# Optimization experiments

Measured on AMD Instinct MI355X. Metric: run time of the kernel, lower is better.

Reference implementation:

```python
import jax, jax.numpy as jnp
import numpy as np
from jax import lax

V, E, H, T = 100000, 256, 256, 8192
FL, FN, NC = 5, 128, 20


def setup_inputs() -> dict:
    key = jax.random.key(0)
    ks = jax.random.split(key, 12)
    s = 0.05
    return {
        "docs": jax.random.randint(ks[0], (1, T), 0, V),
        "docs_length": jnp.array([T]),
        "labels": jax.random.randint(ks[1], (1,), 0, NC),
        "iteration": 0,
        "embed_W": jax.random.uniform(ks[2], (V, E), jnp.float32, -0.1, 0.1),
        "w_ih": jax.random.normal(ks[3], (4 * H, E), jnp.float32) * s,
        "w_hh": jax.random.normal(ks[4], (4 * H, H), jnp.float32) * s,
        "b_ih": jax.random.normal(ks[5], (4 * H,), jnp.float32) * s,
        "b_hh": jax.random.normal(ks[6], (4 * H,), jnp.float32) * s,
        "conv_w": jax.random.normal(ks[7], (FN, 1, FL, H), jnp.float32) * s,
        "conv_b": jax.random.normal(ks[8], (FN,), jnp.float32) * s,
        "logits_w": jax.random.uniform(ks[9], (NC, FN), jnp.float32, -0.1, 0.1),
        "logits_b": jnp.zeros((NC,), jnp.float32),
    }


def _forward(docs, labels, embed_W, w_ih, w_hh, b_ih, b_hh, conv_w, conv_b, logits_w, logits_b):
    # embed -> ReLU (dropout is identity at p=0)
    x = jax.nn.relu(embed_W[docs[0]])  # (T, E)

    b = b_ih + b_hh

    def step(carry, xt):
        h, c = carry
        g = xt @ w_ih.T + h @ w_hh.T + b  # (4H,)
        i, f, gg, o = jnp.split(g, 4)
        i = jax.nn.sigmoid(i)
        f = jax.nn.sigmoid(f)
        gg = jnp.tanh(gg)
        o = jax.nn.sigmoid(o)
        c = f * c + i * gg
        h = o * jnp.tanh(c)
        return (h, c), h

    init = (jnp.zeros((H,), x.dtype), jnp.zeros((H,), x.dtype))
    _, hs = lax.scan(step, init, x)  # (T, H)

    # Conv2d(1, FN, (FL, H)) valid: (1,1,T,H) -> (1,FN,T-FL+1,1)
    feat = lax.conv_general_dilated(
        hs[None, None, :, :], conv_w, window_strides=(1, 1), padding="VALID",
        dimension_numbers=("NCHW", "OIHW", "NCHW"))
    feat = feat[0, :, :, 0] + conv_b[:, None]  # (FN, T-FL+1)

    # AdaptiveMaxPool2d((FN,1)) == max over time
    pooled = jnp.max(feat, axis=1)  # (FN,)

    logits = pooled @ logits_w.T + logits_b  # (NC,)
    logp = jax.nn.log_softmax(logits)
    loss = -logp[labels[0]]
    acc = (jnp.argmax(logp) == labels[0]).astype(jnp.float32)
    return loss, acc


def reference(docs, docs_length, labels, iteration, embed_W, w_ih, w_hh, b_ih, b_hh,
              conv_w, conv_b, logits_w, logits_b):
    return _forward(docs, labels, embed_W, w_ih, w_hh, b_ih, b_hh,
                    conv_w, conv_b, logits_w, logits_b)
```

## Files before the change

### kernel.cpp

```cpp
#include <hip/hip_runtime.h>
#include <math.h>

#define T_LEN 8192

typedef float f32x4 __attribute__((ext_vector_type(4)));
typedef int   i32x8 __attribute__((ext_vector_type(8)));
typedef int   i32x6 __attribute__((ext_vector_type(6)));

#define DPP_MAX(x, ctrl) fmaxf((x), __int_as_float(__builtin_amdgcn_update_dpp(0, __float_as_int(x), (ctrl), 0xF, 0xF, true)))
#define SB() __builtin_amdgcn_sched_barrier(0)

#define BAR_LDS() do { \
    __builtin_amdgcn_sched_barrier(0); \
    asm volatile("s_waitcnt lgkmcnt(0)" ::: "memory"); \
    __builtin_amdgcn_s_barrier(); \
    __builtin_amdgcn_sched_barrier(0); \
} while (0)

__device__ __forceinline__ float fexp2(float x) {
#if __has_builtin(__builtin_amdgcn_exp2f)
    return __builtin_amdgcn_exp2f(x);
#else
    return exp2f(x);
#endif
}
__device__ __forceinline__ float rcp1p(float e) {
    return __builtin_amdgcn_rcpf(1.f + e);
}
__device__ __forceinline__ float fsig_c(float x) {
    x = fminf(30.f, fmaxf(-30.f, x));
    float e = __expf(-x);
    return __builtin_amdgcn_rcpf(1.f + e);
}
__device__ __forceinline__ float ftanh_c(float x) {
    x = fminf(15.f, fmaxf(-15.f, x));
    float e = __expf(-2.f * x);
    return (1.f - e) * __builtin_amdgcn_rcpf(1.f + e);
}

__device__ __forceinline__ unsigned char enc_e4m3(float x) {
#if __has_builtin(__builtin_amdgcn_cvt_pk_fp8_f32)
    int v = __builtin_amdgcn_cvt_pk_fp8_f32(x, 0.f, 0, false);
    return (unsigned char)(v & 0xff);
#else
    unsigned u = __float_as_uint(x);
    unsigned s = (u >> 24) & 0x80u;
    float a = fabsf(x);
    if (a > 448.f) a = 448.f;
    if (a < 9.765625e-4f) return (unsigned char)s;
    int e = ((int)((__float_as_uint(a) >> 23) & 0xffu)) - 127;
    int eu = e < -6 ? -6 : e;
    float ulp = exp2f((float)(eu - 3));
    float q = rintf(a / ulp);
    int mant, ee;
    if (eu == -6 && q < 8.f) { mant = (int)q; ee = 0; }
    else {
        if (q >= 16.f) { q *= 0.5f; eu += 1; }
        mant = (int)q - 8; ee = eu + 7;
        if (ee > 15 || (ee == 15 && mant > 6)) { ee = 15; mant = 6; }
    }
    return (unsigned char)(s | (unsigned)(ee << 3) | (unsigned)mant);
#endif
}
__device__ __forceinline__ unsigned pk4(float a, float b, float c, float d) {
    return (unsigned)enc_e4m3(a) | ((unsigned)enc_e4m3(b) << 8)
         | ((unsigned)enc_e4m3(c) << 16) | ((unsigned)enc_e4m3(d) << 24);
}

__device__ __forceinline__ unsigned enc_e2m3(float x) {
    unsigned s = (__float_as_uint(x) >> 31) << 5;
    float a = fabsf(x);
    a = fminf(a, 7.5f);
    if (a < 0.0625f) return s;
    int e = ((int)((__float_as_uint(a) >> 23) & 0xffu)) - 127;
    int eu = e < 0 ? 0 : e;
    float ulp = __int_as_float((unsigned)(eu + 124) << 23);
    float q = rintf(a * __builtin_amdgcn_rcpf(ulp));
    int E, M;
    if (e < 0) {
        if (q >= 8.f) { E = 1; M = 0; }
        else { E = 0; M = (int)q; }
    } else {
        if (q >= 16.f) { q = 8.f; eu += 1; }
        if (eu > 2) { E = 3; M = 7; }
        else { E = eu + 1; M = (int)q - 8; }
    }
    return s | (unsigned)(E << 3) | (unsigned)M;
}

__device__ __forceinline__ int enc_e2m3_h4(float h) {
    float x = h * 4.f;
    float a = fabsf(x);
    int c1 = (int)rintf(a * 8.f);
    int c2 = (int)rintf(a * 4.f) + 8;
    int mag = (a < 2.f) ? c1 : c2;
    return mag | (int)((__float_as_uint(h) >> 26) & 32u);
}

__global__ __launch_bounds__(256) void pack_w6b(
    const float* __restrict__ w_hh,
    unsigned* __restrict__ w6)
{
    int idx = blockIdx.x * 256 + threadIdx.x;
    int l  = idx & 63;
    int kt = (idx >> 6) & 1;
    int gt = idx >> 7;
    int rw = l & 15, ks = l >> 4;
    int orow = ((rw & 3) << 8) + 64 * (gt >> 4) + (gt & 15) + 16 * (rw >> 2);
    const float* s = w_hh + (size_t)orow * 256 + 128 * kt + 32 * ks;
    unsigned d[6] = {0, 0, 0, 0, 0, 0};
#pragma unroll
    for (int j = 0; j < 32; ++j) {
        unsigned c = enc_e2m3(s[j] * 32.f);
        int bit = 6 * j;
        d[bit >> 5] |= c << (bit & 31);
        if ((bit & 31) > 26) d[(bit >> 5) + 1] |= c >> (32 - (bit & 31));
    }
    unsigned* o = w6 + (size_t)idx * 8;
    o[0] = d[0]; o[1] = d[1]; o[2] = d[2];
    o[3] = d[3]; o[4] = d[4]; o[5] = d[5];
    o[6] = 0;    o[7] = 0;
}

__global__ __launch_bounds__(256, 4) void gemm_pre(
    const int* __restrict__ docs,
    const float* __restrict__ embW,
    const float* __restrict__ w_ih,
    const float* __restrict__ b_ih,
    const float* __restrict__ b_hh,
    float* __restrict__ pre)
{
    __shared__ __align__(16) float As[16][68];
    __shared__ __align__(16) float Bs[16][68];
    __shared__ int rowid[64];
    const int bt = blockIdx.x;
    const int bj = blockIdx.y;
    const int tid = threadIdx.x;
    if (tid < 64) rowid[tid] = docs[bt * 64 + tid];
    __syncthreads();
    const int ti = tid & 15, tj = tid >> 4;
    const int r = tid & 63;
    const int kk4 = (tid >> 6) * 4;
    float acc[4][4];
#pragma unroll
    for (int ii = 0; ii < 4; ++ii)
#pragma unroll
        for (int jj = 0; jj < 4; ++jj) acc[ii][jj] = 0.f;

    for (int k0 = 0; k0 < 256; k0 += 16) {
        float4 av = *(const float4*)(embW + (size_t)rowid[r] * 256 + k0 + kk4);
        float4 bv = *(const float4*)(w_ih + (size_t)(bj * 64 + r) * 256 + k0 + kk4);
        As[kk4 + 0][r] = fmaxf(av.x, 0.f);
        As[kk4 + 1][r] = fmaxf(av.y, 0.f);
        As[kk4 + 2][r] = fmaxf(av.z, 0.f);
        As[kk4 + 3][r] = fmaxf(av.w, 0.f);
        Bs[kk4 + 0][r] = bv.x;
        Bs[kk4 + 1][r] = bv.y;
        Bs[kk4 + 2][r] = bv.z;
        Bs[kk4 + 3][r] = bv.w;
        __syncthreads();
#pragma unroll
        for (int kk = 0; kk < 16; ++kk) {
            float4 a = *(const float4*)&As[kk][ti * 4];
            float4 b = *(const float4*)&Bs[kk][tj * 4];
            acc[0][0] += a.x * b.x; acc[0][1] += a.x * b.y; acc[0][2] += a.x * b.z; acc[0][3] += a.x * b.w;
            acc[1][0] += a.y * b.x; acc[1][1] += a.y * b.y; acc[1][2] += a.y * b.z; acc[1][3] += a.y * b.w;
            acc[2][0] += a.z * b.x; acc[2][1] += a.z * b.y; acc[2][2] += a.z * b.z; acc[2][3] += a.z * b.w;
            acc[3][0] += a.w * b.x; acc[3][1] += a.w * b.y; acc[3][2] += a.w * b.z; acc[3][3] += a.w * b.w;
        }
        __syncthreads();
    }
#pragma unroll
    for (int ii = 0; ii < 4; ++ii) {
        int t = bt * 64 + ti * 4 + ii;
#pragma unroll
        for (int jj = 0; jj < 4; ++jj) {
            int j = bj * 64 + tj * 4 + jj;
            int jp = ((j & 255) << 2) | (j >> 8);
            pre[(size_t)t * 1024 + jp] = acc[ii][jj] + b_ih[j] + b_hh[j];
        }
    }
}

#define MFMA_K0(RT, DST) \
    asm("v_mfma_scale_f32_16x16x128_f8f6f4 %0, %1, %2, %3, %4, %4 cbsz:2 blgp:2" \
        : "=&v"(DST) : "a"(wA[RT][0]), "v"(bq0), "v"(CZ), "v"(sc))
#define MFMA_K1(RT, DST) \
    asm("v_mfma_scale_f32_16x16x128_f8f6f4 %0, %1, %2, %0, %3, %3 cbsz:2 blgp:2" \
        : "+v"(DST) : "a"(wA[RT][1]), "v"(bq1), "v"(sc))

#define MFMA_PAIR(RT, DST) \
    asm("v_mfma_scale_f32_16x16x128_f8f6f4 %0, %1, %2, %5, %6, %6 cbsz:2 blgp:2\n\t" \
        "v_mfma_scale_f32_16x16x128_f8f6f4 %0, %3, %4, %0, %6, %6 cbsz:2 blgp:2" \
        : "=&v"(DST) \
        : "a"(wA[RT][0]), "v"(bq0), "a"(wA[RT][1]), "v"(bq1), "v"(CZ), "v"(sc))

__global__ __launch_bounds__(256, 1) void lstm_scan_mx6c(
    const float* __restrict__ pre,
    const unsigned* __restrict__ w6,
    float* __restrict__ hs)
{
    const int tid = threadIdx.x;
    const int w  = tid >> 6;
    const int l  = tid & 63;
    const int rto = l & 15;
    const int kgr = l >> 4;
    const float C_L2E  = -1.4426950408889634f;
    const float C_L2E2 = -2.8853900817779268f;
    const float I_L2E  = C_L2E  / 128.f;
    const float I_L2E2 = C_L2E2 / 128.f;

    __shared__ __align__(32) unsigned char h6pk[2][256];

    i32x6 wA[16][2];
#pragma unroll
    for (int rtt = 0; rtt < 16; ++rtt) {
#pragma unroll
        for (int kt = 0; kt < 2; ++kt) {
            int gt = 16 * w + rtt;
            const unsigned* s = w6 + (size_t)((gt * 2 + kt) * 64 + l) * 8;
            uint4 lo = *(const uint4*)s;
            uint2 hi = *(const uint2*)(s + 4);
            i32x6 v;
            v[0] = (int)lo.x; v[1] = (int)lo.y; v[2] = (int)lo.z;
            v[3] = (int)lo.w; v[4] = (int)hi.x; v[5] = (int)hi.y;
            wA[rtt][kt] = v;
        }
    }

    for (int i = tid; i < 512; i += 256) ((unsigned char*)h6pk)[i] = 0;

    const int u = 64 * w + rto + 16 * kgr;
    float c_st = 0.f;

    const bool b0 = (rto & 1), b1 = (rto & 2), b2 = (rto & 4), b3 = (rto & 8);

    const int qi  = l & 3;
    const bool iswr = (qi < 3);
    const int rsh = 2 * qi;
    const int qq  = l >> 2;
    const int G   = 4 * (qq >> 2) + (qq & 3);
    const int wofs = (2 * w + (G >> 3)) * 32 + 3 * (G & 7) + qi;

    f32x4 CZ = (f32x4){0.f, 0.f, 0.f, 0.f};
    asm("" : "+v"(CZ));
    int sc = 0x7f7f7f7f;

    f32x4 p4c = *(const f32x4*)(pre + 4 * u);
    float tx = p4c.x * C_L2E;
    float ty = p4c.y * C_L2E;
    float tz = p4c.z * C_L2E2;
    float tw = p4c.w * C_L2E;
    const float* pp = pre + 1024 + 4 * u;
    float* hsp = hs + u;
    const unsigned char* h6base = (const unsigned char*)h6pk;
    BAR_LDS();

#define LSTM_STEP(RD, WR) do { \
    f32x4 p4n = *(const f32x4*)pp; pp += 1024; \
    i32x6 bq0, bq1; \
    { \
        const unsigned char* bp0 = h6base + (RD) + kgr * 32; \
        uint4 lo = *(const uint4*)bp0; \
        uint2 hi = *(const uint2*)(bp0 + 16); \
        bq0[0] = (int)lo.x; bq0[1] = (int)lo.y; bq0[2] = (int)lo.z; \
        bq0[3] = (int)lo.w; bq0[4] = (int)hi.x; bq0[5] = (int)hi.y; \
        const unsigned char* bp1 = bp0 + 128; \
        uint4 lo1 = *(const uint4*)bp1; \
        uint2 hi1 = *(const uint2*)(bp1 + 16); \
        bq1[0] = (int)lo1.x; bq1[1] = (int)lo1.y; bq1[2] = (int)lo1.z; \
        bq1[3] = (int)lo1.w; bq1[4] = (int)hi1.x; bq1[5] = (int)hi1.y; \
    } \
    f32x4 a0, a1, a2, a3, a4, a5, a6, a7, a8, a9, a10, a11, a12, a13, a14, a15; \
    MFMA_K0(0, a0);   MFMA_K0(1, a1);   MFMA_K0(2, a2);   MFMA_K0(3, a3); \
    MFMA_K0(4, a4);   MFMA_K0(5, a5);   MFMA_K0(6, a6);   MFMA_K0(7, a7); \
    MFMA_K0(8, a8);   MFMA_K0(9, a9);   MFMA_K0(10, a10); MFMA_K0(11, a11); \
    MFMA_K0(12, a12); MFMA_K0(13, a13); MFMA_K0(14, a14); MFMA_K0(15, a15); \
    SB(); \
    MFMA_K1(0, a0);   MFMA_K1(1, a1);   MFMA_K1(2, a2);   MFMA_K1(3, a3); \
    MFMA_K1(4, a4);   MFMA_K1(5, a5);   SB(); \
    f32x4 s0 = b0 ? a1 : a0; \
    MFMA_K1(6, a6);   MFMA_K1(7, a7);   SB(); \
    f32x4 s1 = b0 ? a3 : a2; \
    MFMA_K1(8, a8);   MFMA_K1(9, a9);   SB(); \
    f32x4 s2 = b0 ? a5 : a4; \
    f32x4 q0 = b1 ? s1 : s0; \
    MFMA_K1(10, a10); MFMA_K1(11, a11); SB(); \
    f32x4 s3 = b0 ? a7 : a6; \
    MFMA_K1(12, a12); MFMA_K1(13, a13); SB(); \
    f32x4 s4 = b0 ? a9 : a8; \
    MFMA_K1(14, a14); MFMA_K1(15, a15); SB(); \
    f32x4 s5 = b0 ? a11 : a10; \
    f32x4 q1 = b1 ? s3 : s2; \
    asm volatile("s_nop 7\n\ts_nop 7\n\ts_nop 7" : "+v"(a12), "+v"(a13), "+v"(a14), "+v"(a15)); \
    f32x4 s6 = b0 ? a13 : a12; \
    f32x4 s7 = b0 ? a15 : a14; \
    f32x4 q2 = b1 ? s5 : s4; \
    f32x4 q3 = b1 ? s7 : s6; \
    f32x4 r0 = b2 ? q1 : q0; \
    f32x4 r1 = b2 ? q3 : q2; \
    f32x4 av = b3 ? r1 : r0; \
    float nx = p4n.x * C_L2E, ny = p4n.y * C_L2E; \
    float nz = p4n.z * C_L2E2, nw = p4n.w * C_L2E; \
    float si = rcp1p(fexp2(fmaf(av.x, I_L2E,  tx))); \
    float sf = rcp1p(fexp2(fmaf(av.y, I_L2E,  ty))); \
    float tg = 2.f * rcp1p(fexp2(fmaf(av.z, I_L2E2, tz))) - 1.f; \
    float so = rcp1p(fexp2(fmaf(av.w, I_L2E,  tw))); \
    c_st = sf * c_st + si * tg; \
    float h = so * (2.f * rcp1p(fexp2(c_st * C_L2E2)) - 1.f); \
    hsp[0] = h; hsp += 256; \
    int code = enc_e2m3_h4(h); \
    int cnx = __builtin_amdgcn_update_dpp(0, code, 0x39, 0xF, 0xF, true); \
    if (iswr) { \
        unsigned byte = (((unsigned)code >> rsh) | ((unsigned)cnx << (6 - rsh))) & 0xffu; \
        *((unsigned char*)h6pk + (WR) + wofs) = (unsigned char)byte; \
    } \
    tx = nx; ty = ny; tz = nz; tw = nw; \
    BAR_LDS(); \
} while (0)

    for (int t2 = 0; t2 < T_LEN; t2 += 2) {
        LSTM_STEP(256, 0);
        LSTM_STEP(0, 256);
    }
#undef LSTM_STEP
}

__global__ __launch_bounds__(256, 1) void lstm_scan_mx6b(
    const float* __restrict__ pre,
    const unsigned* __restrict__ w6,
    float* __restrict__ hs)
{
    const int tid = threadIdx.x;
    const int w  = tid >> 6;
    const int l  = tid & 63;
    const int rto = l & 15;
    const int kgr = l >> 4;
    const float C_L2E  = -1.4426950408889634f;
    const float C_L2E2 = -2.8853900817779268f;
    const float I_L2E  = C_L2E  / 128.f;
    const float I_L2E2 = C_L2E2 / 128.f;

    __shared__ __align__(32) unsigned char h6pk[2][256];

    i32x6 wA[16][2];
#pragma unroll
    for (int rtt = 0; rtt < 16; ++rtt) {
#pragma unroll
        for (int kt = 0; kt < 2; ++kt) {
            int gt = 16 * w + rtt;
            const unsigned* s = w6 + (size_t)((gt * 2 + kt) * 64 + l) * 8;
            uint4 lo = *(const uint4*)s;
            uint2 hi = *(const uint2*)(s + 4);
            i32x6 v;
            v[0] = (int)lo.x; v[1] = (int)lo.y; v[2] = (int)lo.z;
            v[3] = (int)lo.w; v[4] = (int)hi.x; v[5] = (int)hi.y;
            wA[rtt][kt] = v;
        }
    }

    for (int i = tid; i < 512; i += 256) ((unsigned char*)h6pk)[i] = 0;

    const int u = 64 * w + rto + 16 * kgr;
    float c_st = 0.f;

    const bool b0 = (rto & 1), b1 = (rto & 2), b2 = (rto & 4), b3 = (rto & 8);

    const int qi  = l & 3;
    const bool iswr = (qi < 3);
    const int rsh = 2 * qi;
    const int qq  = l >> 2;
    const int G   = 4 * (qq >> 2) + (qq & 3);
    const int wofs = (2 * w + (G >> 3)) * 32 + 3 * (G & 7) + qi;

    f32x4 CZ = (f32x4){0.f, 0.f, 0.f, 0.f};
    asm("" : "+v"(CZ));
    int sc = 0x7f7f7f7f;

    f32x4 p4c = *(const f32x4*)(pre + 4 * u);
    float tx = p4c.x * C_L2E;
    float ty = p4c.y * C_L2E;
    float tz = p4c.z * C_L2E2;
    float tw = p4c.w * C_L2E;
    const float* pp = pre + 1024 + 4 * u;
    float* hsp = hs + u;
    const unsigned char* h6base = (const unsigned char*)h6pk;
    BAR_LDS();

#define LSTM_STEP(RD, WR) do { \
    f32x4 p4n = *(const f32x4*)pp; pp += 1024; \
    i32x6 bq0, bq1; \
    { \
        const unsigned char* bp0 = h6base + (RD) + kgr * 32; \
        uint4 lo = *(const uint4*)bp0; \
        uint2 hi = *(const uint2*)(bp0 + 16); \
        bq0[0] = (int)lo.x; bq0[1] = (int)lo.y; bq0[2] = (int)lo.z; \
        bq0[3] = (int)lo.w; bq0[4] = (int)hi.x; bq0[5] = (int)hi.y; \
        const unsigned char* bp1 = bp0 + 128; \
        uint4 lo1 = *(const uint4*)bp1; \
        uint2 hi1 = *(const uint2*)(bp1 + 16); \
        bq1[0] = (int)lo1.x; bq1[1] = (int)lo1.y; bq1[2] = (int)lo1.z; \
        bq1[3] = (int)lo1.w; bq1[4] = (int)hi1.x; bq1[5] = (int)hi1.y; \
    } \
    f32x4 a0, a1, a2, a3, a4, a5, a6, a7, a8, a9, a10, a11, a12, a13, a14, a15; \
    MFMA_PAIR(0, a0);  MFMA_PAIR(1, a1);  MFMA_PAIR(2, a2);  MFMA_PAIR(3, a3); \
    SB(); \
    f32x4 s0 = b0 ? a1 : a0; \
    MFMA_PAIR(4, a4);  MFMA_PAIR(5, a5);  SB(); \
    f32x4 s1 = b0 ? a3 : a2; \
    MFMA_PAIR(6, a6);  MFMA_PAIR(7, a7);  SB(); \
    f32x4 s2 = b0 ? a5 : a4; \
    MFMA_PAIR(8, a8);  MFMA_PAIR(9, a9);  SB(); \
    f32x4 s3 = b0 ? a7 : a6; \
    f32x4 q0 = b1 ? s1 : s0; \
    MFMA_PAIR(10, a10); MFMA_PAIR(11, a11); SB(); \
    f32x4 s4 = b0 ? a9 : a8; \
    MFMA_PAIR(12, a12); MFMA_PAIR(13, a13); SB(); \
    f32x4 s5 = b0 ? a11 : a10; \
    f32x4 q1 = b1 ? s3 : s2; \
    MFMA_PAIR(14, a14); MFMA_PAIR(15, a15); SB(); \
    f32x4 s6 = b0 ? a13 : a12; \
    asm volatile("s_nop 7\n\ts_nop 7" : "+v"(a14), "+v"(a15)); \
    f32x4 s7 = b0 ? a15 : a14; \
    f32x4 q2 = b1 ? s5 : s4; \
    f32x4 q3 = b1 ? s7 : s6; \
    f32x4 r0 = b2 ? q1 : q0; \
    f32x4 r1 = b2 ? q3 : q2; \
    f32x4 av = b3 ? r1 : r0; \
    float nx = p4n.x * C_L2E, ny = p4n.y * C_L2E; \
    float nz = p4n.z * C_L2E2, nw = p4n.w * C_L2E; \
    float si = rcp1p(fexp2(fmaf(av.x, I_L2E,  tx))); \
    float sf = rcp1p(fexp2(fmaf(av.y, I_L2E,  ty))); \
    float tg = 2.f * rcp1p(fexp2(fmaf(av.z, I_L2E2, tz))) - 1.f; \
    float so = rcp1p(fexp2(fmaf(av.w, I_L2E,  tw))); \
    c_st = sf * c_st + si * tg; \
    float h = so * (2.f * rcp1p(fexp2(c_st * C_L2E2)) - 1.f); \
    hsp[0] = h; hsp += 256; \
    int code = enc_e2m3_h4(h); \
    int cnx = __builtin_amdgcn_update_dpp(0, code, 0x39, 0xF, 0xF, true); \
    if (iswr) { \
        unsigned byte = (((unsigned)code >> rsh) | ((unsigned)cnx << (6 - rsh))) & 0xffu; \
        *((unsigned char*)h6pk + (WR) + wofs) = (unsigned char)byte; \
    } \
    tx = nx; ty = ny; tz = nz; tw = nw; \
    BAR_LDS(); \
} while (0)

    for (int t2 = 0; t2 < T_LEN; t2 += 2) {
        LSTM_STEP(256, 0);
        LSTM_STEP(0, 256);
    }
#undef LSTM_STEP
}

__global__ __launch_bounds__(512, 2) void lstm_scan_mx8(
    const float* __restrict__ pre,
    const float* __restrict__ w_hh,
    float* __restrict__ hs)
{
    const int tid = threadIdx.x;
    const int w  = tid >> 6;
    const int l  = tid & 63;
    const int rw = l & 15;
    const int kg = l >> 4;
    const float INV = 1.f / 32768.f;

    __shared__ __align__(16) unsigned char h8[2 * 256];
    __shared__ __align__(16) float ldsPre[2][1024];

    i32x8 wA[8][2];
#pragma unroll
    for (int rt = 0; rt < 8; ++rt) {
#pragma unroll
        for (int kt = 0; kt < 2; ++kt) {
            int rowp = ((8 * w + rt) << 4) + rw;
            int orow = ((rowp & 3) << 8) + (rowp >> 2);
            const float* s = w_hh + (size_t)orow * 256 + 128 * kt + 32 * kg;
            i32x8 v;
#pragma unroll
            for (int d = 0; d < 8; ++d) {
                float4 f = *(const float4*)(s + 4 * d);
                v[d] = (int)pk4(f.x * 512.f, f.y * 512.f, f.z * 512.f, f.w * 512.f);
            }
            wA[rt][kt] = v;
        }
    }

    for (int i = tid; i < 512; i += 512) h8[i] = 0;
    {
        float2 p = *(const float2*)(pre + 2 * tid);
        *(float2*)&ldsPre[0][2 * tid] = p;
    }
    float c_st = 0.f;
    const bool isup = (rw < 8);
    const int u = 32 * w + 4 * (rw & 7) + kg;
    const float* pnext = pre + 1024 + 2 * tid;
    float* hsp = hs + u;
    __syncthreads();

    for (int t = 0; t < T_LEN; ++t) {
        const int PW = t & 1;
        const int PR = PW ^ 1;

        f32x4 p4 = *(const f32x4*)&ldsPre[PW][4 * u];

        float2 pv = *(const float2*)pnext;
        if (t + 2 < T_LEN) pnext += 1024;

        i32x8 bq[2];
#pragma unroll
        for (int kt = 0; kt < 2; ++kt) {
            const unsigned char* bp = &h8[PR * 256 + 128 * kt + 32 * kg];
            uint4 lo = *(const uint4*)bp;
            uint4 hi = *(const uint4*)(bp + 16);
            i32x8 b;
            b[0] = (int)lo.x; b[1] = (int)lo.y; b[2] = (int)lo.z; b[3] = (int)lo.w;
            b[4] = (int)hi.x; b[5] = (int)hi.y; b[6] = (int)hi.z; b[7] = (int)hi.w;
            bq[kt] = b;
        }

        f32x4 acc[8];
#pragma unroll
        for (int rt = 0; rt < 8; ++rt) acc[rt] = (f32x4){0.f, 0.f, 0.f, 0.f};
#pragma unroll
        for (int rt = 0; rt < 8; ++rt)
#pragma unroll
            for (int kt = 0; kt < 2; ++kt)
                acc[rt] = __builtin_amdgcn_mfma_scale_f32_16x16x128_f8f6f4(
                    wA[rt][kt], bq[kt], acc[rt],
                    0, 0, 0, 0x7f7f7f7f, 0, 0x7f7f7f7f);

        if (isup) {
            f32x4 av = acc[0];
            av = (rw == 1) ? acc[1] : av;
            av = (rw == 2) ? acc[2] : av;
            av = (rw == 3) ? acc[3] : av;
            av = (rw == 4) ? acc[4] : av;
            av = (rw == 5) ? acc[5] : av;
            av = (rw == 6) ? acc[6] : av;
            av = (rw == 7) ? acc[7] : av;
            float gi = fmaf(av.x, INV, p4.x);
            float gf = fmaf(av.y, INV, p4.y);
            float gg = fmaf(av.z, INV, p4.z);
            float go = fmaf(av.w, INV, p4.w);
            float si = fsig_c(gi);
            float sf = fsig_c(gf);
            float tg = ftanh_c(gg);
            float so = fsig_c(go);
            c_st = sf * c_st + si * tg;
            float h = so * ftanh_c(c_st);
            hsp[0] = h;
            h8[PW * 256 + u] = enc_e4m3(h * 64.f);
        }
        hsp += 256;

        *(float2*)&ldsPre[PR][2 * tid] = pv;

        __syncthreads();
    }
}

__global__ __launch_bounds__(256) void conv_pool(
    const float* __restrict__ hs,
    const float* __restrict__ cw,
    const float* __restrict__ cb,
    float* __restrict__ part)
{
    __shared__ __align__(16) float hst[68 * 260];
    __shared__ __align__(16) float cwS[128 * 68];
    const int blk = blockIdx.x;
    const int t0 = blk * 64;
    const int tid = threadIdx.x;
    const int i = tid & 15;
    const int g = tid >> 4;

    for (int e = tid; e < 68 * 64; e += 256) {
        int rr = e >> 6;
        int c4 = (e & 63) * 4;
        int tg = t0 + rr; if (tg > 8191) tg = 8191;
        float4 v = *(const float4*)(hs + (size_t)tg * 256 + c4);
        *(float4*)&hst[rr * 260 + c4] = v;
    }

    float acc[4][8];
#pragma unroll
    for (int tt = 0; tt < 4; ++tt)
#pragma unroll
        for (int j = 0; j < 8; ++j) acc[tt][j] = 0.f;

    for (int l = 0; l < 5; ++l) {
        for (int hc = 0; hc < 4; ++hc) {
            __syncthreads();
            {
                int n = tid >> 1;
                int hb = (tid & 1) * 32;
                const float* src = cw + (size_t)n * 1280 + l * 256 + hc * 64 + hb;
                float* dst = &cwS[n * 68 + hb];
#pragma unroll
                for (int q = 0; q < 8; ++q) {
                    float4 v = *(const float4*)(src + 4 * q);
                    *(float4*)(dst + 4 * q) = v;
                }
            }
            __syncthreads();
#pragma unroll 4
            for (int q = 0; q < 16; ++q) {
                float4 hvv[4];
#pragma unroll
                for (int tt = 0; tt < 4; ++tt)
                    hvv[tt] = *(const float4*)&hst[(i + 16 * tt + l) * 260 + hc * 64 + 4 * q];
#pragma unroll
                for (int j = 0; j < 8; ++j) {
                    float4 wv = *(const float4*)&cwS[(g + 16 * j) * 68 + 4 * q];
#pragma unroll
                    for (int tt = 0; tt < 4; ++tt) {
                        acc[tt][j] += hvv[tt].x * wv.x + hvv[tt].y * wv.y
                                    + hvv[tt].z * wv.z + hvv[tt].w * wv.w;
                    }
                }
            }
        }
    }

    float m[8];
#pragma unroll
    for (int j = 0; j < 8; ++j) {
        int n = g + 16 * j;
        float cbn = cb[n];
        float mm = -INFINITY;
#pragma unroll
        for (int tt = 0; tt < 4; ++tt) {
            int t = t0 + i + 16 * tt;
            float v = acc[tt][j] + cbn;
            if (t < 8188) mm = fmaxf(mm, v);
        }
        mm = DPP_MAX(mm, 0xB1);
        mm = DPP_MAX(mm, 0x4E);
        mm = DPP_MAX(mm, 0x141);
        mm = DPP_MAX(mm, 0x140);
        m[j] = mm;
    }
    if (i == 0) {
#pragma unroll
        for (int j = 0; j < 8; ++j)
            part[(size_t)blk * 128 + g + 16 * j] = m[j];
    }
}

__global__ void final_head(
    const float* __restrict__ part,
    const float* __restrict__ logits_w,
    const float* __restrict__ logits_b,
    const int* __restrict__ labels,
    float* __restrict__ out)
{
    __shared__ float pooled[128];
    __shared__ float lgt[20];
    int tid = threadIdx.x;
    float mx = -INFINITY;
    for (int b = 0; b < 128; ++b) mx = fmaxf(mx, part[(size_t)b * 128 + tid]);
    pooled[tid] = mx;
    __syncthreads();
    if (tid < 20) {
        float s = logits_b[tid];
        for (int k = 0; k < 128; ++k) s += logits_w[tid * 128 + k] * pooled[k];
        lgt[tid] = s;
    }
    __syncthreads();
    if (tid == 0) {
        float m = lgt[0]; int am = 0;
        for (int c2 = 1; c2 < 20; ++c2) { if (lgt[c2] > m) { m = lgt[c2]; am = c2; } }
        float se = 0.f;
        for (int c2 = 0; c2 < 20; ++c2) se += expf(lgt[c2] - m);
        float lse = m + logf(se);
        int lbl = labels[0];
        out[0] = -(lgt[lbl] - lse);
        out[1] = (am == lbl) ? 1.f : 0.f;
    }
}

extern "C" void kernel_launch(void* const* d_in, const int* in_sizes, int n_in,
                              void* d_out, int out_size, void* d_ws, size_t ws_size,
                              hipStream_t stream) {
    (void)in_sizes; (void)n_in; (void)out_size;
    const int*   docs   = (const int*)d_in[0];
    const int*   labels = (const int*)d_in[2];
    const float* embW   = (const float*)d_in[4];
    const float* w_ih   = (const float*)d_in[5];
    const float* w_hh   = (const float*)d_in[6];
    const float* b_ih   = (const float*)d_in[7];
    const float* b_hh   = (const float*)d_in[8];
    const float* cw     = (const float*)d_in[9];
    const float* cb     = (const float*)d_in[10];
    const float* lw     = (const float*)d_in[11];
    const float* lb     = (const float*)d_in[12];
    float* out = (float*)d_out;

    char* ws = (char*)d_ws;
    float*    pre  = (float*)(ws);
    float*    hs   = (float*)(ws + 33554432);
    float*    part = (float*)(ws + 41943040);
    unsigned* w6   = (unsigned*)(ws + 42008576);

    bool ws_ok = (ws_size >= (size_t)42270720);
    hipFuncAttributes aC, aB;
    bool okC = ws_ok
        && (hipFuncGetAttributes(&aC, (const void*)lstm_scan_mx6c) == hipSuccess)
        && (aC.localSizeBytes == 0);
    bool okB = ws_ok
        && (hipFuncGetAttributes(&aB, (const void*)lstm_scan_mx6b) == hipSuccess)
        && (aB.localSizeBytes == 0);

    gemm_pre<<<dim3(128, 16, 1), 256, 0, stream>>>(docs, embW, w_ih, b_ih, b_hh, pre);
    if (okC) {
        pack_w6b<<<32, 256, 0, stream>>>(w_hh, w6);
        lstm_scan_mx6c<<<1, 256, 0, stream>>>(pre, w6, hs);
    } else if (okB) {
        pack_w6b<<<32, 256, 0, stream>>>(w_hh, w6);
        lstm_scan_mx6b<<<1, 256, 0, stream>>>(pre, w6, hs);
    } else {
        lstm_scan_mx8<<<1, 512, 0, stream>>>(pre, w_hh, hs);
    }
    conv_pool<<<128, 256, 0, stream>>>(hs, cw, cb, part);
    final_head<<<1, 128, 0, stream>>>(part, lw, lb, labels, out);
}
```

Measured before the change: 5.300 ms.

## Split LSTM recurrent scan across 8 wavefronts with half the gate tiles each

Replaces the 4-wave serial LSTM scan kernel with an 8-wave (512-thread) version in which each wave holds 8 instead of 16 weight row-tiles and issues half as many MFMA pairs per timestep. Two waves now share each hidden-unit group, and only the owning half of lanes writes hs and the packed h bytes. The aim is to shorten the per-step MFMA critical path in the latency-bound recurrence. The cost is more waves joining the per-step barrier and duplicated activation math on the non-owning lanes.

```diff
diff --git a/kernel.cpp b/kernel.cpp
--- a/kernel.cpp
+++ b/kernel.cpp
@@ -182,20 +182,13 @@
     }
 }
 
-#define MFMA_K0(RT, DST) \
-    asm("v_mfma_scale_f32_16x16x128_f8f6f4 %0, %1, %2, %3, %4, %4 cbsz:2 blgp:2" \
-        : "=&v"(DST) : "a"(wA[RT][0]), "v"(bq0), "v"(CZ), "v"(sc))
-#define MFMA_K1(RT, DST) \
-    asm("v_mfma_scale_f32_16x16x128_f8f6f4 %0, %1, %2, %0, %3, %3 cbsz:2 blgp:2" \
-        : "+v"(DST) : "a"(wA[RT][1]), "v"(bq1), "v"(sc))
-
 #define MFMA_PAIR(RT, DST) \
     asm("v_mfma_scale_f32_16x16x128_f8f6f4 %0, %1, %2, %5, %6, %6 cbsz:2 blgp:2\n\t" \
         "v_mfma_scale_f32_16x16x128_f8f6f4 %0, %3, %4, %0, %6, %6 cbsz:2 blgp:2" \
         : "=&v"(DST) \
         : "a"(wA[RT][0]), "v"(bq0), "a"(wA[RT][1]), "v"(bq1), "v"(CZ), "v"(sc))
 
-__global__ __launch_bounds__(256, 1) void lstm_scan_mx6c(
+__global__ __launch_bounds__(512, 2) void lstm_scan_mx6d(
     const float* __restrict__ pre,
     const unsigned* __restrict__ w6,
     float* __restrict__ hs)
@@ -212,7 +205,128 @@
 
     __shared__ __align__(32) unsigned char h6pk[2][256];
 
-    i32x6 wA[16][2];
+    i32x6 wA[8][2];
+#pragma unroll
+    for (int rtt = 0; rtt < 8; ++rtt) {
+#pragma unroll
+        for (int kt = 0; kt < 2; ++kt) {
+            int gt = 8 * w + rtt;
+            const unsigned* s = w6 + (size_t)((gt * 2 + kt) * 64 + l) * 8;
+            uint4 lo = *(const uint4*)s;
+            uint2 hi = *(const uint2*)(s + 4);
+            i32x6 v;
+            v[0] = (int)lo.x; v[1] = (int)lo.y; v[2] = (int)lo.z;
+            v[3] = (int)lo.w; v[4] = (int)hi.x; v[5] = (int)hi.y;
+            wA[rtt][kt] = v;
+        }
+    }
+
+    for (int i = tid; i < 512; i += 512) ((unsigned char*)h6pk)[i] = 0;
+
+    const bool isown = (rto < 8);
+    const int u = 64 * (w >> 1) + 8 * (w & 1) + (rto & 7) + 16 * kgr;
+    float c_st = 0.f;
+
+    const bool b0 = (rto & 1), b1 = (rto & 2), b2 = (rto & 4);
+
+    const int qi  = l & 3;
+    const bool iswr = ((l & 8) == 0) && (qi < 3);
+    const int rsh = 2 * qi;
+    const int wofs = (u >> 5) * 32 + 3 * ((u & 31) >> 2) + qi;
+
+    f32x4 CZ = (f32x4){0.f, 0.f, 0.f, 0.f};
+    asm("" : "+v"(CZ));
+    int sc = 0x7f7f7f7f;
+
+    f32x4 p4c = *(const f32x4*)(pre + 4 * u);
+    float tx = p4c.x * C_L2E;
+    float ty = p4c.y * C_L2E;
+    float tz = p4c.z * C_L2E2;
+    float tw = p4c.w * C_L2E;
+    const float* pp = pre + 1024 + 4 * u;
+    float* hsp = hs + u;
+    const unsigned char* h6base = (const unsigned char*)h6pk;
+    BAR_LDS();
+
+#define LSTM_STEP(RD, WR) do { \
+    f32x4 p4n = *(const f32x4*)pp; pp += 1024; \
+    i32x6 bq0, bq1; \
+    { \
+        const unsigned char* bp0 = h6base + (RD) + kgr * 32; \
+        uint4 lo = *(const uint4*)bp0; \
+        uint2 hi = *(const uint2*)(bp0 + 16); \
+        bq0[0] = (int)lo.x; bq0[1] = (int)lo.y; bq0[2] = (int)lo.z; \
+        bq0[3] = (int)lo.w; bq0[4] = (int)hi.x; bq0[5] = (int)hi.y; \
+        const unsigned char* bp1 = bp0 + 128; \
+        uint4 lo1 = *(const uint4*)bp1; \
+        uint2 hi1 = *(const uint2*)(bp1 + 16); \
+        bq1[0] = (int)lo1.x; bq1[1] = (int)lo1.y; bq1[2] = (int)lo1.z; \
+        bq1[3] = (int)lo1.w; bq1[4] = (int)hi1.x; bq1[5] = (int)hi1.y; \
+    } \
+    f32x4 a0, a1, a2, a3, a4, a5, a6, a7; \
+    MFMA_PAIR(0, a0);  MFMA_PAIR(1, a1);  MFMA_PAIR(2, a2);  MFMA_PAIR(3, a3); \
+    SB(); \
+    f32x4 s0 = b0 ? a1 : a0; \
+    MFMA_PAIR(4, a4);  MFMA_PAIR(5, a5);  SB(); \
+    f32x4 s1 = b0 ? a3 : a2; \
+    MFMA_PAIR(6, a6);  MFMA_PAIR(7, a7);  SB(); \
+    f32x4 s2 = b0 ? a5 : a4; \
+    f32x4 q0 = b1 ? s1 : s0; \
+    asm volatile("s_nop 7\n\ts_nop 7" : "+v"(a6), "+v"(a7)); \
+    f32x4 s3 = b0 ? a7 : a6; \
+    f32x4 q1 = b1 ? s3 : s2; \
+    f32x4 av = b2 ? q1 : q0; \
+    float nx = p4n.x * C_L2E, ny = p4n.y * C_L2E; \
+    float nz = p4n.z * C_L2E2, nw = p4n.w * C_L2E; \
+    float si = rcp1p(fexp2(fmaf(av.x, I_L2E,  tx))); \
+    float sf = rcp1p(fexp2(fmaf(av.y, I_L2E,  ty))); \
+    float tg = 2.f * rcp1p(fexp2(fmaf(av.z, I_L2E2, tz))) - 1.f; \
+    float so = rcp1p(fexp2(fmaf(av.w, I_L2E,  tw))); \
+    c_st = sf * c_st + si * tg; \
+    float h = so * (2.f * rcp1p(fexp2(c_st * C_L2E2)) - 1.f); \
+    if (isown) hsp[0] = h; \
+    hsp += 256; \
+    int code = enc_e2m3_h4(h); \
+    int cnx = __builtin_amdgcn_update_dpp(0, code, 0x39, 0xF, 0xF, true); \
+    if (iswr) { \
+        unsigned byte = (((unsigned)code >> rsh) | ((unsigned)cnx << (6 - rsh))) & 0xffu; \
+        *((unsigned char*)h6pk + (WR) + wofs) = (unsigned char)byte; \
+    } \
+    tx = nx; ty = ny; tz = nz; tw = nw; \
+    BAR_LDS(); \
+} while (0)
+
+    for (int t2 = 0; t2 < T_LEN; t2 += 2) {
+        LSTM_STEP(256, 0);
+        LSTM_STEP(0, 256);
+    }
+#undef LSTM_STEP
+}
+
+#define MFMA_PAIR16(RT, DST) \
+    asm("v_mfma_scale_f32_16x16x128_f8f6f4 %0, %1, %2, %5, %6, %6 cbsz:2 blgp:2\n\t" \
+        "v_mfma_scale_f32_16x16x128_f8f6f4 %0, %3, %4, %0, %6, %6 cbsz:2 blgp:2" \
+        : "=&v"(DST) \
+        : "a"(wB[RT][0]), "v"(bq0), "a"(wB[RT][1]), "v"(bq1), "v"(CZ), "v"(sc))
+
+__global__ __launch_bounds__(256, 1) void lstm_scan_mx6b(
+    const float* __restrict__ pre,
+    const unsigned* __restrict__ w6,
+    float* __restrict__ hs)
+{
+    const int tid = threadIdx.x;
+    const int w  = tid >> 6;
+    const int l  = tid & 63;
+    const int rto = l & 15;
+    const int kgr = l >> 4;
+    const float C_L2E  = -1.4426950408889634f;
+    const float C_L2E2 = -2.8853900817779268f;
+    const float I_L2E  = C_L2E  / 128.f;
+    const float I_L2E2 = C_L2E2 / 128.f;
+
+    __shared__ __align__(32) unsigned char h6pk[2][256];
+
+    i32x6 wB[16][2];
 #pragma unroll
     for (int rtt = 0; rtt < 16; ++rtt) {
 #pragma unroll
@@ -224,7 +338,7 @@
             i32x6 v;
             v[0] = (int)lo.x; v[1] = (int)lo.y; v[2] = (int)lo.z;
             v[3] = (int)lo.w; v[4] = (int)hi.x; v[5] = (int)hi.y;
-            wA[rtt][kt] = v;
+            wB[rtt][kt] = v;
         }
     }
 
@@ -272,153 +386,22 @@
         bq1[3] = (int)lo1.w; bq1[4] = (int)hi1.x; bq1[5] = (int)hi1.y; \
     } \
     f32x4 a0, a1, a2, a3, a4, a5, a6, a7, a8, a9, a10, a11, a12, a13, a14, a15; \
-    MFMA_K0(0, a0);   MFMA_K0(1, a1);   MFMA_K0(2, a2);   MFMA_K0(3, a3); \
-    MFMA_K0(4, a4);   MFMA_K0(5, a5);   MFMA_K0(6, a6);   MFMA_K0(7, a7); \
-    MFMA_K0(8, a8);   MFMA_K0(9, a9);   MFMA_K0(10, a10); MFMA_K0(11, a11); \
-    MFMA_K0(12, a12); MFMA_K0(13, a13); MFMA_K0(14, a14); MFMA_K0(15, a15); \
+    MFMA_PAIR16(0, a0);  MFMA_PAIR16(1, a1);  MFMA_PAIR16(2, a2);  MFMA_PAIR16(3, a3); \
     SB(); \
-    MFMA_K1(0, a0);   MFMA_K1(1, a1);   MFMA_K1(2, a2);   MFMA_K1(3, a3); \
-    MFMA_K1(4, a4);   MFMA_K1(5, a5);   SB(); \
     f32x4 s0 = b0 ? a1 : a0; \
-    MFMA_K1(6, a6);   MFMA_K1(7, a7);   SB(); \
+    MFMA_PAIR16(4, a4);  MFMA_PAIR16(5, a5);  SB(); \
     f32x4 s1 = b0 ? a3 : a2; \
-    MFMA_K1(8, a8);   MFMA_K1(9, a9);   SB(); \
+    MFMA_PAIR16(6, a6);  MFMA_PAIR16(7, a7);  SB(); \
     f32x4 s2 = b0 ? a5 : a4; \
+    MFMA_PAIR16(8, a8);  MFMA_PAIR16(9, a9);  SB(); \
+    f32x4 s3 = b0 ? a7 : a6; \
     f32x4 q0 = b1 ? s1 : s0; \
-    MFMA_K1(10, a10); MFMA_K1(11, a11); SB(); \
-    f32x4 s3 = b0 ? a7 : a6; \
-    MFMA_K1(12, a12); MFMA_K1(13, a13); SB(); \
+    MFMA_PAIR16(10, a10); MFMA_PAIR16(11, a11); SB(); \
     f32x4 s4 = b0 ? a9 : a8; \
-    MFMA_K1(14, a14); MFMA_K1(15, a15); SB(); \
+    MFMA_PAIR16(12, a12); MFMA_PAIR16(13, a13); SB(); \
     f32x4 s5 = b0 ? a11 : a10; \
     f32x4 q1 = b1 ? s3 : s2; \
-    asm volatile("s_nop 7\n\ts_nop 7\n\ts_nop 7" : "+v"(a12), "+v"(a13), "+v"(a14), "+v"(a15)); \
-    f32x4 s6 = b0 ? a13 : a12; \
-    f32x4 s7 = b0 ? a15 : a14; \
-    f32x4 q2 = b1 ? s5 : s4; \
-    f32x4 q3 = b1 ? s7 : s6; \
-    f32x4 r0 = b2 ? q1 : q0; \
-    f32x4 r1 = b2 ? q3 : q2; \
-    f32x4 av = b3 ? r1 : r0; \
-    float nx = p4n.x * C_L2E, ny = p4n.y * C_L2E; \
-    float nz = p4n.z * C_L2E2, nw = p4n.w * C_L2E; \
-    float si = rcp1p(fexp2(fmaf(av.x, I_L2E,  tx))); \
-    float sf = rcp1p(fexp2(fmaf(av.y, I_L2E,  ty))); \
-    float tg = 2.f * rcp1p(fexp2(fmaf(av.z, I_L2E2, tz))) - 1.f; \
-    float so = rcp1p(fexp2(fmaf(av.w, I_L2E,  tw))); \
-    c_st = sf * c_st + si * tg; \
-    float h = so * (2.f * rcp1p(fexp2(c_st * C_L2E2)) - 1.f); \
-    hsp[0] = h; hsp += 256; \
-    int code = enc_e2m3_h4(h); \
-    int cnx = __builtin_amdgcn_update_dpp(0, code, 0x39, 0xF, 0xF, true); \
-    if (iswr) { \
-        unsigned byte = (((unsigned)code >> rsh) | ((unsigned)cnx << (6 - rsh))) & 0xffu; \
-        *((unsigned char*)h6pk + (WR) + wofs) = (unsigned char)byte; \
-    } \
-    tx = nx; ty = ny; tz = nz; tw = nw; \
-    BAR_LDS(); \
-} while (0)
-
-    for (int t2 = 0; t2 < T_LEN; t2 += 2) {
-        LSTM_STEP(256, 0);
-        LSTM_STEP(0, 256);
-    }
-#undef LSTM_STEP
-}
-
-__global__ __launch_bounds__(256, 1) void lstm_scan_mx6b(
-    const float* __restrict__ pre,
-    const unsigned* __restrict__ w6,
-    float* __restrict__ hs)
-{
-    const int tid = threadIdx.x;
-    const int w  = tid >> 6;
-    const int l  = tid & 63;
-    const int rto = l & 15;
-    const int kgr = l >> 4;
-    const float C_L2E  = -1.4426950408889634f;
-    const float C_L2E2 = -2.8853900817779268f;
-    const float I_L2E  = C_L2E  / 128.f;
-    const float I_L2E2 = C_L2E2 / 128.f;
-
-    __shared__ __align__(32) unsigned char h6pk[2][256];
-
-    i32x6 wA[16][2];
-#pragma unroll
-    for (int rtt = 0; rtt < 16; ++rtt) {
-#pragma unroll
-        for (int kt = 0; kt < 2; ++kt) {
-            int gt = 16 * w + rtt;
-            const unsigned* s = w6 + (size_t)((gt * 2 + kt) * 64 + l) * 8;
-            uint4 lo = *(const uint4*)s;
-            uint2 hi = *(const uint2*)(s + 4);
-            i32x6 v;
-            v[0] = (int)lo.x; v[1] = (int)lo.y; v[2] = (int)lo.z;
-            v[3] = (int)lo.w; v[4] = (int)hi.x; v[5] = (int)hi.y;
-            wA[rtt][kt] = v;
-        }
-    }
-
-    for (int i = tid; i < 512; i += 256) ((unsigned char*)h6pk)[i] = 0;
-
-    const int u = 64 * w + rto + 16 * kgr;
-    float c_st = 0.f;
-
-    const bool b0 = (rto & 1), b1 = (rto & 2), b2 = (rto & 4), b3 = (rto & 8);
-
-    const int qi  = l & 3;
-    const bool iswr = (qi < 3);
-    const int rsh = 2 * qi;
-    const int qq  = l >> 2;
-    const int G   = 4 * (qq >> 2) + (qq & 3);
-    const int wofs = (2 * w + (G >> 3)) * 32 + 3 * (G & 7) + qi;
-
-    f32x4 CZ = (f32x4){0.f, 0.f, 0.f, 0.f};
-    asm("" : "+v"(CZ));
-    int sc = 0x7f7f7f7f;
-
-    f32x4 p4c = *(const f32x4*)(pre + 4 * u);
-    float tx = p4c.x * C_L2E;
-    float ty = p4c.y * C_L2E;
-    float tz = p4c.z * C_L2E2;
-    float tw = p4c.w * C_L2E;
-    const float* pp = pre + 1024 + 4 * u;
-    float* hsp = hs + u;
-    const unsigned char* h6base = (const unsigned char*)h6pk;
-    BAR_LDS();
-
-#define LSTM_STEP(RD, WR) do { \
-    f32x4 p4n = *(const f32x4*)pp; pp += 1024; \
-    i32x6 bq0, bq1; \
-    { \
-        const unsigned char* bp0 = h6base + (RD) + kgr * 32; \
-        uint4 lo = *(const uint4*)bp0; \
-        uint2 hi = *(const uint2*)(bp0 + 16); \
-        bq0[0] = (int)lo.x; bq0[1] = (int)lo.y; bq0[2] = (int)lo.z; \
-        bq0[3] = (int)lo.w; bq0[4] = (int)hi.x; bq0[5] = (int)hi.y; \
-        const unsigned char* bp1 = bp0 + 128; \
-        uint4 lo1 = *(const uint4*)bp1; \
-        uint2 hi1 = *(const uint2*)(bp1 + 16); \
-        bq1[0] = (int)lo1.x; bq1[1] = (int)lo1.y; bq1[2] = (int)lo1.z; \
-        bq1[3] = (int)lo1.w; bq1[4] = (int)hi1.x; bq1[5] = (int)hi1.y; \
-    } \
-    f32x4 a0, a1, a2, a3, a4, a5, a6, a7, a8, a9, a10, a11, a12, a13, a14, a15; \
-    MFMA_PAIR(0, a0);  MFMA_PAIR(1, a1);  MFMA_PAIR(2, a2);  MFMA_PAIR(3, a3); \
-    SB(); \
-    f32x4 s0 = b0 ? a1 : a0; \
-    MFMA_PAIR(4, a4);  MFMA_PAIR(5, a5);  SB(); \
-    f32x4 s1 = b0 ? a3 : a2; \
-    MFMA_PAIR(6, a6);  MFMA_PAIR(7, a7);  SB(); \
-    f32x4 s2 = b0 ? a5 : a4; \
-    MFMA_PAIR(8, a8);  MFMA_PAIR(9, a9);  SB(); \
-    f32x4 s3 = b0 ? a7 : a6; \
-    f32x4 q0 = b1 ? s1 : s0; \
-    MFMA_PAIR(10, a10); MFMA_PAIR(11, a11); SB(); \
-    f32x4 s4 = b0 ? a9 : a8; \
-    MFMA_PAIR(12, a12); MFMA_PAIR(13, a13); SB(); \
-    f32x4 s5 = b0 ? a11 : a10; \
-    f32x4 q1 = b1 ? s3 : s2; \
-    MFMA_PAIR(14, a14); MFMA_PAIR(15, a15); SB(); \
+    MFMA_PAIR16(14, a14); MFMA_PAIR16(15, a15); SB(); \
     f32x4 s6 = b0 ? a13 : a12; \
     asm volatile("s_nop 7\n\ts_nop 7" : "+v"(a14), "+v"(a15)); \
     f32x4 s7 = b0 ? a15 : a14; \
@@ -703,18 +686,18 @@
     unsigned* w6   = (unsigned*)(ws + 42008576);
 
     bool ws_ok = (ws_size >= (size_t)42270720);
-    hipFuncAttributes aC, aB;
-    bool okC = ws_ok
-        && (hipFuncGetAttributes(&aC, (const void*)lstm_scan_mx6c) == hipSuccess)
-        && (aC.localSizeBytes == 0);
+    hipFuncAttributes aD, aB;
+    bool okD = ws_ok
+        && (hipFuncGetAttributes(&aD, (const void*)lstm_scan_mx6d) == hipSuccess)
+        && (aD.localSizeBytes == 0);
     bool okB = ws_ok
         && (hipFuncGetAttributes(&aB, (const void*)lstm_scan_mx6b) == hipSuccess)
         && (aB.localSizeBytes == 0);
 
     gemm_pre<<<dim3(128, 16, 1), 256, 0, stream>>>(docs, embW, w_ih, b_ih, b_hh, pre);
-    if (okC) {
+    if (okD) {
         pack_w6b<<<32, 256, 0, stream>>>(w_hh, w6);
-        lstm_scan_mx6c<<<1, 256, 0, stream>>>(pre, w6, hs);
+        lstm_scan_mx6d<<<1, 512, 0, stream>>>(pre, w6, hs);
     } else if (okB) {
         pack_w6b<<<32, 256, 0, stream>>>(w_hh, w6);
         lstm_scan_mx6b<<<1, 256, 0, stream>>>(pre, w6, hs);
```

New measurement: 5.111 ms. 1.04x faster.
